# Performance work log

Hardware: AMD Instinct MI355X
Metric: run time of the kernel (lower is better)

The kernel has to match this reference:

```python
import jax, jax.numpy as jnp
import numpy as np

HIDDEN = 256
NUM_STEPS = 3
N_NODES = 200000
N_GRAPHS = 512


def setup_inputs() -> dict:
    key = jax.random.key(0)
    ks = jax.random.split(key, 8)
    h = HIDDEN
    x = jax.random.normal(ks[0], (N_NODES, h), dtype=jnp.float32)
    batch = jnp.sort(jax.random.randint(ks[1], (N_NODES,), 0, N_GRAPHS)).astype(jnp.int64)
    s_ih = 1.0 / np.sqrt(2 * h)
    s_hh = 1.0 / np.sqrt(h)
    # LSTM (input 2h -> hidden h), PyTorch gate order i,f,g,o
    W_ih = jax.random.uniform(ks[2], (4 * h, 2 * h), jnp.float32, -s_ih, s_ih)
    W_hh = jax.random.uniform(ks[3], (4 * h, h), jnp.float32, -s_hh, s_hh)
    b_ih = jax.random.uniform(ks[4], (4 * h,), jnp.float32, -s_hh, s_hh)
    b_hh = jax.random.uniform(ks[5], (4 * h,), jnp.float32, -s_hh, s_hh)
    # out_proj: Linear(2h -> h)
    s_o = 1.0 / np.sqrt(2 * h)
    W_out = jax.random.uniform(ks[6], (h, 2 * h), jnp.float32, -s_o, s_o)
    b_out = jax.random.uniform(ks[7], (h,), jnp.float32, -s_o, s_o)
    return {"x": x, "batch": batch, "W_ih": W_ih, "W_hh": W_hh,
            "b_ih": b_ih, "b_hh": b_hh, "W_out": W_out, "b_out": b_out,
            "n_graphs": N_GRAPHS}


def _set2set(x, batch, W_ih, W_hh, b_ih, b_hh, n_graphs):
    h = x.shape[1]
    hs = jnp.zeros((n_graphs, h), x.dtype)
    cs = jnp.zeros((n_graphs, h), x.dtype)
    q_star = jnp.zeros((n_graphs, 2 * h), x.dtype)
    for _ in range(NUM_STEPS):
        # LSTM step (PyTorch gate order: i, f, g, o)
        gates = q_star @ W_ih.T + hs @ W_hh.T + (b_ih + b_hh)  # [B, 4h]
        i_g, f_g, g_g, o_g = jnp.split(gates, 4, axis=-1)
        cs = jax.nn.sigmoid(f_g) * cs + jax.nn.sigmoid(i_g) * jnp.tanh(g_g)
        hs = jax.nn.sigmoid(o_g) * jnp.tanh(cs)
        q = hs  # [B, h]
        # attention logits per node
        e = jnp.sum(x * q[batch], axis=-1)  # [N]
        # segment softmax over nodes of each graph
        m = jax.ops.segment_max(e, batch, num_segments=n_graphs)
        a = jnp.exp(e - m[batch])
        denom = jax.ops.segment_sum(a, batch, num_segments=n_graphs)
        a = a / denom[batch]
        # weighted readout
        r = jax.ops.segment_sum(a[:, None] * x, batch, num_segments=n_graphs)  # [B, h]
        q_star = jnp.concatenate([q, r], axis=-1)  # [B, 2h]
    return q_star


def reference(x, batch, W_ih, W_hh, b_ih, b_hh, W_out, b_out, n_graphs):
    q_star = _set2set(x, batch.astype(jnp.int32), W_ih, W_hh, b_ih, b_hh, n_graphs)
    return q_star @ W_out.T + b_out
```

## Files before the change

### kernel.cpp

```cpp
#include <hip/hip_runtime.h>
#include <hip/hip_bf16.h>

#define HID 256
#define NG 512
#define CHUNK 32

__device__ __forceinline__ float sigmoidf_(float v) { return 1.f / (1.f + __expf(-v)); }

__device__ __forceinline__ void load_lds16(const void* g, void* l) {
    __builtin_amdgcn_global_load_lds(
        (const __attribute__((address_space(1))) void*)g,
        (__attribute__((address_space(3))) void*)l, 16, 0, 0);
}

__global__ __launch_bounds__(256) void prep_kernel(
    const float* __restrict__ W_ih, const float* __restrict__ W_hh,
    const float* __restrict__ b_ih, const float* __restrict__ b_hh,
    float* __restrict__ Wcat, float* __restrict__ bcat)
{
    int idx = blockIdx.x * 256 + threadIdx.x;
    if (idx < 1024 * 512) {
        int k = idx & 511;
        float v = W_ih[idx];
        if (k < 256) v += W_hh[(idx >> 9) * 256 + k];
        Wcat[idx] = v;
    }
    if (idx < 1024) bcat[idx] = b_ih[idx] + b_hh[idx];
}

__global__ __launch_bounds__(256) void find_starts(
    const int* __restrict__ batch, int n, int* __restrict__ starts)
{
    int g = blockIdx.x * 256 + threadIdx.x;
    if (g > NG) return;
    if (g == NG) { starts[NG] = n; return; }
    int lo = 0, hi = n;
    while (lo < hi) {
        int mid = (lo + hi) >> 1;
        if (batch[mid] < g) lo = mid + 1; else hi = mid;
    }
    starts[g] = lo;
}

__global__ __launch_bounds__(256) void attn_kernel(
    const float* __restrict__ x, const int* __restrict__ starts,
    const float* __restrict__ gp0, const float* __restrict__ gp1,
    const float* __restrict__ bcat, float* __restrict__ cs,
    float* __restrict__ qs, int step0)
{
    __shared__ __align__(16) float xl[2][CHUNK * HID];
    __shared__ __align__(16) float ql[HID];
    __shared__ float e_arr[CHUNK];

    const int g = blockIdx.x;
    const int tid = threadIdx.x;
    const int lane = tid & 63;

    float ig, fg, gg, og, cp;
    if (step0) {
        ig = bcat[tid]; fg = bcat[256 + tid]; gg = bcat[512 + tid]; og = bcat[768 + tid];
        cp = 0.f;
    } else {
        const float* a0 = gp0 + (size_t)g * 1024;
        const float* a1 = gp1 + (size_t)g * 1024;
        ig = a0[tid]       + a1[tid]       + bcat[tid];
        fg = a0[256 + tid] + a1[256 + tid] + bcat[256 + tid];
        gg = a0[512 + tid] + a1[512 + tid] + bcat[512 + tid];
        og = a0[768 + tid] + a1[768 + tid] + bcat[768 + tid];
        cp = cs[g * HID + tid];
    }
    float cn = sigmoidf_(fg) * cp + sigmoidf_(ig) * tanhf(gg);
    float h  = sigmoidf_(og) * tanhf(cn);
    cs[g * HID + tid] = cn;
    qs[(size_t)g * 512 + tid] = h;
    ql[tid] = h;

    const int s0 = starts[g];
    const int nn = starts[g + 1] - s0;
    if (nn <= 0) { qs[(size_t)g * 512 + HID + tid] = 0.f; return; }

    const int j = tid >> 3;
    const int s = tid & 7;
    const int row = lane & 31;
    const int w = tid >> 6;

    const int nchunks = (nn + CHUNK - 1) / CHUNK;
    const int tail = nn - (nchunks - 1) * CHUNK;

    if (nchunks <= 2 && tail < CHUNK) {
        float4 z = make_float4(0.f, 0.f, 0.f, 0.f);
        int base = (nchunks - 1) & 1;
        int cnt = (CHUNK - tail) * HID;
        for (int off = tid * 4; off < cnt; off += 1024)
            *(float4*)&xl[base][tail * HID + off] = z;
    }

    const char* src = (const char*)x + (size_t)s0 * 1024;

    {
        int bytes = (nn < CHUNK ? nn : CHUNK) * 1024;
        #pragma unroll
        for (int i = 0; i < 8; ++i) {
            int offw = i * 4096 + w * 1024;
            int offc = offw < bytes - 1024 ? offw : bytes - 1024;
            load_lds16(src + offc + lane * 16, (char*)&xl[0][0] + offw + lane * 16);
        }
    }
    asm volatile("s_waitcnt lgkmcnt(0)\n\ts_barrier" ::: "memory");

    float4 qf[8];
    #pragma unroll
    for (int k = 0; k < 8; ++k) qf[k] = *(const float4*)&ql[k * 32 + s * 4];

    float m_run = -3.402823466e38f, l_run = 0.f;
    float4 racc[8] = {};

    for (int c = 0; c < nchunks; ++c) {
        const int buf = c & 1;
        int rem = nn - c * CHUNK;
        const int nnc = rem < CHUNK ? rem : CHUNK;
        if (c + 1 < nchunks) {
            const char* src2 = src + (size_t)(c + 1) * (CHUNK * 1024);
            int rem2 = nn - (c + 1) * CHUNK;
            int bytes = (rem2 < CHUNK ? rem2 : CHUNK) * 1024;
            char* dst = (char*)&xl[buf ^ 1][0];
            #pragma unroll
            for (int i = 0; i < 8; ++i) {
                int offw = i * 4096 + w * 1024;
                int offc = offw < bytes - 1024 ? offw : bytes - 1024;
                load_lds16(src2 + offc + lane * 16, dst + offw + lane * 16);
            }
            asm volatile("s_waitcnt vmcnt(8)" ::: "memory");
        } else {
            asm volatile("s_waitcnt vmcnt(0)" ::: "memory");
        }
        asm volatile("s_barrier" ::: "memory");

        const float* xb = &xl[buf][0];
        float4 xr[8];
        #pragma unroll
        for (int k = 0; k < 8; ++k) xr[k] = *(const float4*)&xb[j * HID + k * 32 + s * 4];

        float e = 0.f;
        #pragma unroll
        for (int k = 0; k < 8; ++k)
            e += xr[k].x * qf[k].x + xr[k].y * qf[k].y + xr[k].z * qf[k].z + xr[k].w * qf[k].w;
        e += __shfl_xor(e, 1); e += __shfl_xor(e, 2); e += __shfl_xor(e, 4);
        if (s == 0) e_arr[j] = e;
        asm volatile("s_waitcnt lgkmcnt(0)\n\ts_barrier" ::: "memory");

        float eL = (row < nnc) ? e_arr[row] : -3.402823466e38f;
        float mc = eL;
        #pragma unroll
        for (int o = 16; o; o >>= 1) mc = fmaxf(mc, __shfl_xor(mc, o));
        float m_new = fmaxf(m_run, mc);
        float alpha = __expf(m_run - m_new);
        float pL = (row < nnc) ? __expf(eL - m_new) : 0.f;
        float ps = pL;
        #pragma unroll
        for (int o = 16; o; o >>= 1) ps += __shfl_xor(ps, o);
        l_run = l_run * alpha + ps;
        m_run = m_new;
        float p = __shfl(pL, j);

        #pragma unroll
        for (int k = 0; k < 8; ++k) {
            racc[k].x = racc[k].x * alpha + p * xr[k].x;
            racc[k].y = racc[k].y * alpha + p * xr[k].y;
            racc[k].z = racc[k].z * alpha + p * xr[k].z;
            racc[k].w = racc[k].w * alpha + p * xr[k].w;
        }
    }

    asm volatile("s_waitcnt lgkmcnt(0)\n\ts_barrier" ::: "memory");
    float* red = &xl[0][0];
    #pragma unroll
    for (int k = 0; k < 8; ++k)
        *(float4*)&red[j * HID + k * 32 + s * 4] = racc[k];
    asm volatile("s_waitcnt lgkmcnt(0)\n\ts_barrier" ::: "memory");
    float sum = 0.f;
    #pragma unroll
    for (int jj = 0; jj < 32; ++jj) sum += red[jj * HID + tid];
    qs[(size_t)g * 512 + HID + tid] = sum / l_run;
}

__global__ __launch_bounds__(256) void gemm_splitk(
    const float* __restrict__ A, int lda,
    const float* __restrict__ B, int ldb,
    float* __restrict__ Cp, int ldc, int KS, size_t slice_stride)
{
    __shared__ float As[16][76];
    __shared__ float Bs[16][76];
    const int tid = threadIdx.x;
    const int tx = tid & 15, ty = tid >> 4;
    const int m0 = blockIdx.y * 64, n0 = blockIdx.x * 64;
    const int kb = blockIdx.z * KS;
    const int r = tid >> 2, kc = (tid & 3) << 2;
    float acc[4][4] = {};

    const float* Ap = &A[(size_t)(m0 + r) * lda + kb + kc];
    const float* Bp = &B[(size_t)(n0 + r) * ldb + kb + kc];
    float4 av = *(const float4*)Ap;
    float4 bv = *(const float4*)Bp;

    for (int k0 = 0; k0 < KS; k0 += 16) {
        As[kc + 0][r] = av.x; As[kc + 1][r] = av.y; As[kc + 2][r] = av.z; As[kc + 3][r] = av.w;
        Bs[kc + 0][r] = bv.x; Bs[kc + 1][r] = bv.y; Bs[kc + 2][r] = bv.z; Bs[kc + 3][r] = bv.w;
        __syncthreads();
        if (k0 + 16 < KS) {
            av = *(const float4*)(Ap + k0 + 16);
            bv = *(const float4*)(Bp + k0 + 16);
        }
        #pragma unroll
        for (int kk = 0; kk < 16; ++kk) {
            float4 a = *(const float4*)&As[kk][ty << 2];
            float4 b = *(const float4*)&Bs[kk][tx << 2];
            acc[0][0] += a.x * b.x; acc[0][1] += a.x * b.y; acc[0][2] += a.x * b.z; acc[0][3] += a.x * b.w;
            acc[1][0] += a.y * b.x; acc[1][1] += a.y * b.y; acc[1][2] += a.y * b.z; acc[1][3] += a.y * b.w;
            acc[2][0] += a.z * b.x; acc[2][1] += a.z * b.y; acc[2][2] += a.z * b.z; acc[2][3] += a.z * b.w;
            acc[3][0] += a.w * b.x; acc[3][1] += a.w * b.y; acc[3][2] += a.w * b.z; acc[3][3] += a.w * b.w;
        }
        __syncthreads();
    }
    float* out = Cp + blockIdx.z * slice_stride;
    #pragma unroll
    for (int i = 0; i < 4; ++i) {
        float4 o = make_float4(acc[i][0], acc[i][1], acc[i][2], acc[i][3]);
        *(float4*)&out[(size_t)(m0 + ty * 4 + i) * ldc + n0 + (tx << 2)] = o;
    }
}

__global__ __launch_bounds__(256) void finalize_out(
    const float* __restrict__ op, const float* __restrict__ b_out,
    float* __restrict__ out)
{
    int i = blockIdx.x * 256 + threadIdx.x;
    if (i < 512 * 256) {
        float v = op[i] + op[131072 + i] + op[262144 + i] + op[393216 + i] + b_out[i & 255];
        out[i] = v;
    }
}

extern "C" void kernel_launch(void* const* d_in, const int* in_sizes, int n_in,
                              void* d_out, int out_size, void* d_ws, size_t ws_size,
                              hipStream_t stream)
{
    const float* x     = (const float*)d_in[0];
    const int*   batch = (const int*)d_in[1];
    const float* W_ih  = (const float*)d_in[2];
    const float* W_hh  = (const float*)d_in[3];
    const float* b_ih  = (const float*)d_in[4];
    const float* b_hh  = (const float*)d_in[5];
    const float* W_out = (const float*)d_in[6];
    const float* b_out = (const float*)d_in[7];
    float* out = (float*)d_out;
    const int n = in_sizes[1];
    (void)n_in; (void)out_size; (void)ws_size;

    char* ws = (char*)d_ws;
    float* qs      = (float*)(ws);
    float* cs      = (float*)(ws + 0x100000);
    float* gates_p = (float*)(ws + 0x180000);
    float* Wcat    = (float*)(ws + 0x580000);
    float* bcat    = (float*)(ws + 0x780000);
    int*   starts  = (int*)  (ws + 0x781000);
    float* out_p   = (float*)(ws + 0x790000);

    prep_kernel<<<2048, 256, 0, stream>>>(W_ih, W_hh, b_ih, b_hh, Wcat, bcat);
    find_starts<<<3, 256, 0, stream>>>(batch, n, starts);

    for (int step = 0; step < 3; ++step) {
        if (step > 0) {
            gemm_splitk<<<dim3(16, 8, 2), 256, 0, stream>>>(
                qs, 512, Wcat, 512, gates_p, 1024, 256, (size_t)512 * 1024);
        }
        attn_kernel<<<NG, 256, 0, stream>>>(
            x, starts, gates_p, gates_p + (size_t)512 * 1024, bcat, cs, qs, step == 0);
    }
    gemm_splitk<<<dim3(4, 8, 4), 256, 0, stream>>>(
        qs, 512, W_out, 512, out_p, 256, 128, (size_t)512 * 256);
    finalize_out<<<512, 256, 0, stream>>>(out_p, b_out, out);
}
```

Measured before the change: 420.3 us.

## Replace LDS double-buffered attention with per-wave register-prefetched online softmax

The attention kernel no longer stages 32-node chunks of x into LDS with global_load_lds and block-wide barriers. Each of the four waves now independently processes 8-node chunks in a strided pattern, prefetching the next chunk into registers while computing the current one. Softmax and readout state are kept per wave using shuffles, and the four partial results are merged at the end with a log-sum-exp rescale. This removes the per-chunk barriers and LDS traffic. In exchange it doubles register usage for x (current and next), and each block has less data in flight per wave than the 32KB LDS staging provided.

```diff
diff --git a/kernel.cpp b/kernel.cpp
--- a/kernel.cpp
+++ b/kernel.cpp
@@ -3,15 +3,8 @@
 
 #define HID 256
 #define NG 512
-#define CHUNK 32
 
 __device__ __forceinline__ float sigmoidf_(float v) { return 1.f / (1.f + __expf(-v)); }
-
-__device__ __forceinline__ void load_lds16(const void* g, void* l) {
-    __builtin_amdgcn_global_load_lds(
-        (const __attribute__((address_space(1))) void*)g,
-        (__attribute__((address_space(3))) void*)l, 16, 0, 0);
-}
 
 __global__ __launch_bounds__(256) void prep_kernel(
     const float* __restrict__ W_ih, const float* __restrict__ W_hh,
@@ -48,13 +41,12 @@
     const float* __restrict__ bcat, float* __restrict__ cs,
     float* __restrict__ qs, int step0)
 {
-    __shared__ __align__(16) float xl[2][CHUNK * HID];
     __shared__ __align__(16) float ql[HID];
-    __shared__ float e_arr[CHUNK];
+    __shared__ __align__(16) float red[4][HID];
+    __shared__ float mw[4], lw[4];
 
     const int g = blockIdx.x;
     const int tid = threadIdx.x;
-    const int lane = tid & 63;
 
     float ig, fg, gg, og, cp;
     if (step0) {
@@ -78,110 +70,97 @@
     const int s0 = starts[g];
     const int nn = starts[g + 1] - s0;
     if (nn <= 0) { qs[(size_t)g * 512 + HID + tid] = 0.f; return; }
-
-    const int j = tid >> 3;
-    const int s = tid & 7;
-    const int row = lane & 31;
-    const int w = tid >> 6;
-
-    const int nchunks = (nn + CHUNK - 1) / CHUNK;
-    const int tail = nn - (nchunks - 1) * CHUNK;
-
-    if (nchunks <= 2 && tail < CHUNK) {
-        float4 z = make_float4(0.f, 0.f, 0.f, 0.f);
-        int base = (nchunks - 1) & 1;
-        int cnt = (CHUNK - tail) * HID;
-        for (int off = tid * 4; off < cnt; off += 1024)
-            *(float4*)&xl[base][tail * HID + off] = z;
-    }
-
-    const char* src = (const char*)x + (size_t)s0 * 1024;
-
-    {
-        int bytes = (nn < CHUNK ? nn : CHUNK) * 1024;
-        #pragma unroll
-        for (int i = 0; i < 8; ++i) {
-            int offw = i * 4096 + w * 1024;
-            int offc = offw < bytes - 1024 ? offw : bytes - 1024;
-            load_lds16(src + offc + lane * 16, (char*)&xl[0][0] + offw + lane * 16);
-        }
-    }
-    asm volatile("s_waitcnt lgkmcnt(0)\n\ts_barrier" ::: "memory");
+    __syncthreads();
+
+    const int w = tid >> 6, lane = tid & 63;
+    const int j = lane >> 3;
+    const int s = lane & 7;
 
     float4 qf[8];
     #pragma unroll
     for (int k = 0; k < 8; ++k) qf[k] = *(const float4*)&ql[k * 32 + s * 4];
 
-    float m_run = -3.402823466e38f, l_run = 0.f;
+    const int nch = (nn + 7) >> 3;
+    const int last = s0 + nn - 1;
+    const float NEG = -3.402823466e38f;
+
+    float m_run = NEG, l_run = 0.f;
     float4 racc[8] = {};
-
-    for (int c = 0; c < nchunks; ++c) {
-        const int buf = c & 1;
-        int rem = nn - c * CHUNK;
-        const int nnc = rem < CHUNK ? rem : CHUNK;
-        if (c + 1 < nchunks) {
-            const char* src2 = src + (size_t)(c + 1) * (CHUNK * 1024);
-            int rem2 = nn - (c + 1) * CHUNK;
-            int bytes = (rem2 < CHUNK ? rem2 : CHUNK) * 1024;
-            char* dst = (char*)&xl[buf ^ 1][0];
+    float4 xc[8], xn[8];
+
+    int c = w;
+    if (c < nch) {
+        int node = s0 + c * 8 + j; if (node > last) node = last;
+        const float* bp = x + (size_t)node * HID + s * 4;
+        #pragma unroll
+        for (int k = 0; k < 8; ++k) xc[k] = *(const float4*)(bp + k * 32);
+    }
+    for (; c < nch; c += 4) {
+        if (c + 4 < nch) {
+            int node = s0 + (c + 4) * 8 + j; if (node > last) node = last;
+            const float* bp = x + (size_t)node * HID + s * 4;
             #pragma unroll
-            for (int i = 0; i < 8; ++i) {
-                int offw = i * 4096 + w * 1024;
-                int offc = offw < bytes - 1024 ? offw : bytes - 1024;
-                load_lds16(src2 + offc + lane * 16, dst + offw + lane * 16);
-            }
-            asm volatile("s_waitcnt vmcnt(8)" ::: "memory");
-        } else {
-            asm volatile("s_waitcnt vmcnt(0)" ::: "memory");
-        }
-        asm volatile("s_barrier" ::: "memory");
-
-        const float* xb = &xl[buf][0];
-        float4 xr[8];
-        #pragma unroll
-        for (int k = 0; k < 8; ++k) xr[k] = *(const float4*)&xb[j * HID + k * 32 + s * 4];
+            for (int k = 0; k < 8; ++k) xn[k] = *(const float4*)(bp + k * 32);
+        }
+        const bool valid = (c * 8 + j) < nn;
 
         float e = 0.f;
         #pragma unroll
         for (int k = 0; k < 8; ++k)
-            e += xr[k].x * qf[k].x + xr[k].y * qf[k].y + xr[k].z * qf[k].z + xr[k].w * qf[k].w;
+            e += xc[k].x * qf[k].x + xc[k].y * qf[k].y + xc[k].z * qf[k].z + xc[k].w * qf[k].w;
         e += __shfl_xor(e, 1); e += __shfl_xor(e, 2); e += __shfl_xor(e, 4);
-        if (s == 0) e_arr[j] = e;
-        asm volatile("s_waitcnt lgkmcnt(0)\n\ts_barrier" ::: "memory");
-
-        float eL = (row < nnc) ? e_arr[row] : -3.402823466e38f;
-        float mc = eL;
-        #pragma unroll
-        for (int o = 16; o; o >>= 1) mc = fmaxf(mc, __shfl_xor(mc, o));
+        e = valid ? e : NEG;
+
+        float mc = e;
+        mc = fmaxf(mc, __shfl_xor(mc, 8));
+        mc = fmaxf(mc, __shfl_xor(mc, 16));
+        mc = fmaxf(mc, __shfl_xor(mc, 32));
         float m_new = fmaxf(m_run, mc);
         float alpha = __expf(m_run - m_new);
-        float pL = (row < nnc) ? __expf(eL - m_new) : 0.f;
-        float ps = pL;
-        #pragma unroll
-        for (int o = 16; o; o >>= 1) ps += __shfl_xor(ps, o);
+        float p = valid ? __expf(e - m_new) : 0.f;
+        float ps = p;
+        ps += __shfl_xor(ps, 8); ps += __shfl_xor(ps, 16); ps += __shfl_xor(ps, 32);
         l_run = l_run * alpha + ps;
         m_run = m_new;
-        float p = __shfl(pL, j);
-
         #pragma unroll
         for (int k = 0; k < 8; ++k) {
-            racc[k].x = racc[k].x * alpha + p * xr[k].x;
-            racc[k].y = racc[k].y * alpha + p * xr[k].y;
-            racc[k].z = racc[k].z * alpha + p * xr[k].z;
-            racc[k].w = racc[k].w * alpha + p * xr[k].w;
-        }
-    }
-
-    asm volatile("s_waitcnt lgkmcnt(0)\n\ts_barrier" ::: "memory");
-    float* red = &xl[0][0];
+            racc[k].x = racc[k].x * alpha + p * xc[k].x;
+            racc[k].y = racc[k].y * alpha + p * xc[k].y;
+            racc[k].z = racc[k].z * alpha + p * xc[k].z;
+            racc[k].w = racc[k].w * alpha + p * xc[k].w;
+        }
+        #pragma unroll
+        for (int k = 0; k < 8; ++k) xc[k] = xn[k];
+    }
+
     #pragma unroll
-    for (int k = 0; k < 8; ++k)
-        *(float4*)&red[j * HID + k * 32 + s * 4] = racc[k];
-    asm volatile("s_waitcnt lgkmcnt(0)\n\ts_barrier" ::: "memory");
-    float sum = 0.f;
-    #pragma unroll
-    for (int jj = 0; jj < 32; ++jj) sum += red[jj * HID + tid];
-    qs[(size_t)g * 512 + HID + tid] = sum / l_run;
+    for (int k = 0; k < 8; ++k) {
+        racc[k].x += __shfl_xor(racc[k].x, 8);
+        racc[k].y += __shfl_xor(racc[k].y, 8);
+        racc[k].z += __shfl_xor(racc[k].z, 8);
+        racc[k].w += __shfl_xor(racc[k].w, 8);
+        racc[k].x += __shfl_xor(racc[k].x, 16);
+        racc[k].y += __shfl_xor(racc[k].y, 16);
+        racc[k].z += __shfl_xor(racc[k].z, 16);
+        racc[k].w += __shfl_xor(racc[k].w, 16);
+        racc[k].x += __shfl_xor(racc[k].x, 32);
+        racc[k].y += __shfl_xor(racc[k].y, 32);
+        racc[k].z += __shfl_xor(racc[k].z, 32);
+        racc[k].w += __shfl_xor(racc[k].w, 32);
+    }
+    if (j == 0) {
+        #pragma unroll
+        for (int k = 0; k < 8; ++k) *(float4*)&red[w][k * 32 + s * 4] = racc[k];
+        if (s == 0) { mw[w] = m_run; lw[w] = l_run; }
+    }
+    __syncthreads();
+
+    float M = fmaxf(fmaxf(mw[0], mw[1]), fmaxf(mw[2], mw[3]));
+    float f0 = __expf(mw[0] - M), f1 = __expf(mw[1] - M);
+    float f2 = __expf(mw[2] - M), f3 = __expf(mw[3] - M);
+    float L = lw[0] * f0 + lw[1] * f1 + lw[2] * f2 + lw[3] * f3;
+    float r = red[0][tid] * f0 + red[1][tid] * f1 + red[2][tid] * f2 + red[3][tid] * f3;
+    qs[(size_t)g * 512 + HID + tid] = r / L;
 }
 
 __global__ __launch_bounds__(256) void gemm_splitk(
```

Result: no change. 413.5 us (-1.6%).
